# Kernel optimization log

Measured on AMD Instinct MI355X. Metric: run time of the kernel, lower is better.

Reference implementation:

```python
import jax, jax.numpy as jnp
import numpy as np

N, D, H, E = 50000, 64, 4, 400000
LN_EPS = 1e-5


def setup_inputs() -> dict:
    key = jax.random.key(0)
    ks = jax.random.split(key, 8)
    x = jax.random.normal(ks[0], (N, D), dtype=jnp.float32)
    edge_index = jax.random.randint(ks[1], (2, E), 0, N, dtype=jnp.int64)
    # nn.Linear(dim, dim*heads, bias=False): weight shape (H*D, D)
    W_lin = jax.random.normal(ks[2], (H * D, D), dtype=jnp.float32) * (1.0 / np.sqrt(D))
    attn_src = jax.random.normal(ks[3], (H, D), dtype=jnp.float32) * 0.1
    attn_dst = jax.random.normal(ks[4], (H, D), dtype=jnp.float32) * 0.1
    # nn.Linear(dim*heads, dim): weight (D, H*D), bias (D,)
    W_out = jax.random.normal(ks[5], (D, H * D), dtype=jnp.float32) * (1.0 / np.sqrt(H * D))
    b_out = jnp.zeros((D,), dtype=jnp.float32)
    ln_g = jnp.ones((D,), dtype=jnp.float32)
    ln_b = jnp.zeros((D,), dtype=jnp.float32)
    return {"x": x, "edge_index": edge_index, "W_lin": W_lin,
            "attn_src": attn_src, "attn_dst": attn_dst,
            "W_out": W_out, "b_out": b_out, "ln_g": ln_g, "ln_b": ln_b}


def reference(x, edge_index, W_lin, attn_src, attn_dst, W_out, b_out, ln_g, ln_b):
    n = x.shape[0]
    i, j = edge_index[0], edge_index[1]  # dst, src node ids per edge
    xh = (x @ W_lin.T).reshape(n, H, D)                 # [N,H,D]
    # per-node attention contributions (equivalent to per-edge dot in source)
    s_dst = jnp.einsum('nhd,hd->nh', xh, attn_dst)      # [N,H]
    s_src = jnp.einsum('nhd,hd->nh', xh, attn_src)      # [N,H]
    alpha = jax.nn.leaky_relu(s_dst[i] + s_src[j], 0.2) # [E,H]
    alpha_exp = jnp.exp(alpha)                          # source uses raw exp (no max-shift)
    denom = jax.ops.segment_sum(alpha_exp, i, num_segments=n)  # [N,H]
    attn = alpha_exp / (denom[i] + 1e-9)                # [E,H]
    msg = attn[:, :, None] * xh[j]                      # [E,H,D]
    out = jax.ops.segment_sum(msg, i, num_segments=n)   # [N,H,D]
    out = out.reshape(n, H * D) @ W_out.T + b_out       # [N,D]
    y = jax.nn.elu(out) + x
    mu = jnp.mean(y, axis=-1, keepdims=True)
    var = jnp.mean(jnp.square(y - mu), axis=-1, keepdims=True)
    return (y - mu) * jax.lax.rsqrt(var + LN_EPS) * ln_g + ln_b
```

## Files before the change

### kernel.cpp

```cpp
#include <hip/hip_runtime.h>

#define N_NODES 50000
#define DIM     64
#define HEADS   4
#define NEDGES  400000
#define HD      256
#define MAXDEG  32
#define NPREP   256
#define ZSTRIDE 264

typedef _Float16 half2v __attribute__((ext_vector_type(2)));
typedef _Float16 half4v __attribute__((ext_vector_type(4)));
typedef _Float16 half8v __attribute__((ext_vector_type(8)));
typedef float    f32x4  __attribute__((ext_vector_type(4)));

union EU { int2 i2; half4v h; };

__global__ __launch_bounds__(256) void k_prep(
    const float* __restrict__ x,
    const float* __restrict__ W_lin,
    const float* __restrict__ attn_src,
    const float* __restrict__ attn_dst,
    const float* __restrict__ W_out,
    const int* __restrict__ ei,
    _Float16* __restrict__ G2T,
    _Float16* __restrict__ x16,
    float* __restrict__ S,
    int* __restrict__ cnt,
    int* __restrict__ bucketJ)
{
    __shared__ float weffsh[512];
    const int b = blockIdx.x, t = threadIdx.x;

    for (int e = b * 256 + t; e < NEDGES; e += NPREP * 256) {
        const int i = ei[e];
        const int j = ei[NEDGES + e];
        const int slot = atomicAdd(&cnt[i], 1);
        if (slot < MAXDEG) bucketJ[(size_t)i * MAXDEG + slot] = j;
    }

    for (int id = t; id < 512; id += 256) {
        const int sd = id >> 8, rem = id & 255, h = rem >> 6, k = rem & 63;
        const float* av = sd ? attn_dst : attn_src;
        float acc = 0.f;
        for (int d = 0; d < DIM; ++d)
            acc = fmaf(av[h * DIM + d], W_lin[(h * DIM + d) * DIM + k], acc);
        weffsh[id] = acc;
    }

    {
        const int id = b * 256 + t;
        if (id < 64 * 256) {
            const int d = id >> 8, rem = id & 255, m = rem >> 2, h = rem & 3;
            float acc = 0.f;
            for (int k = 0; k < DIM; ++k)
                acc = fmaf(W_lin[(h * DIM + k) * DIM + m],
                           W_out[d * HD + h * DIM + k], acc);
            G2T[d * HD + m * 4 + h] = (_Float16)acc;
        }
    }
    __syncthreads();

    for (int base = b * 32; base < N_NODES; base += NPREP * 32) {
        const int ni = base + (t >> 3);
        if (ni < N_NODES) {
            const int combo = t & 7;
            const float4* xr = (const float4*)(x + (size_t)ni * DIM);
            const float4* wr = (const float4*)(weffsh + combo * DIM);
            float acc = 0.f;
#pragma unroll
            for (int kp = 0; kp < 16; ++kp) {
                const float4 a = xr[kp], bw = wr[kp];
                acc = fmaf(a.x, bw.x, acc);
                acc = fmaf(a.y, bw.y, acc);
                acc = fmaf(a.z, bw.z, acc);
                acc = fmaf(a.w, bw.w, acc);
            }
            S[(size_t)ni * 8 + combo] = acc;
        }
        const size_t e0 = (size_t)base * DIM + (size_t)t * 8;
        if (e0 + 8 <= (size_t)N_NODES * DIM) {
            const float4 u = *(const float4*)(x + e0);
            const float4 v = *(const float4*)(x + e0 + 4);
            half8v hv;
            hv[0]=(_Float16)u.x; hv[1]=(_Float16)u.y; hv[2]=(_Float16)u.z; hv[3]=(_Float16)u.w;
            hv[4]=(_Float16)v.x; hv[5]=(_Float16)v.y; hv[6]=(_Float16)v.z; hv[7]=(_Float16)v.w;
            *(half8v*)(x16 + e0) = hv;
        }
    }
}

__global__ __launch_bounds__(256) void k_ga(
    const int* __restrict__ cnt,
    const int* __restrict__ bucketJ,
    const float* __restrict__ S,
    const _Float16* __restrict__ x16,
    const _Float16* __restrict__ G2T,
    const float* __restrict__ b_out,
    const float* __restrict__ ln_g,
    const float* __restrict__ ln_b,
    float* __restrict__ out)
{
    __shared__ _Float16 znsh[16 * ZSTRIDE];
    __shared__ float ysh[16][65];

    const int t = threadIdx.x, wv = t >> 6, l = t & 63;
    const int n0 = blockIdx.x * 16;
    const int side = l >> 5, p = l & 31;

    const int4 degv = *(const int4*)(cnt + n0 + wv * 4);
    int degc[4];
    degc[0] = degv.x < MAXDEG ? degv.x : MAXDEG;
    degc[1] = degv.y < MAXDEG ? degv.y : MAXDEG;
    degc[2] = degv.z < MAXDEG ? degv.z : MAXDEG;
    degc[3] = degv.w < MAXDEG ? degv.w : MAXDEG;

    int Jr[4];
#pragma unroll
    for (int r = 0; r < 4; ++r)
        Jr[r] = bucketJ[(size_t)(n0 + wv * 4 + r) * MAXDEG + p];
#pragma unroll
    for (int r = 0; r < 4; ++r)
        Jr[r] = (p < degc[r]) ? Jr[r] : 0;

    float4 SSr[4], SDr[4];
#pragma unroll
    for (int r = 0; r < 4; ++r)
        SSr[r] = *(const float4*)(S + (size_t)Jr[r] * 8);
#pragma unroll
    for (int r = 0; r < 4; ++r)
        SDr[r] = *(const float4*)(S + (size_t)(n0 + wv * 4 + r) * 8 + 4);

    int Ey[4], Ez[4];
#pragma unroll
    for (int r = 0; r < 4; ++r) {
        float u;
        u = SDr[r].x + SSr[r].x; u = u > 0.f ? u : 0.2f * u; const float e0 = __expf(u);
        u = SDr[r].y + SSr[r].y; u = u > 0.f ? u : 0.2f * u; const float e1 = __expf(u);
        u = SDr[r].z + SSr[r].z; u = u > 0.f ? u : 0.2f * u; const float e2 = __expf(u);
        u = SDr[r].w + SSr[r].w; u = u > 0.f ? u : 0.2f * u; const float e3 = __expf(u);
        EU pk;
        pk.h[0] = (_Float16)e0; pk.h[1] = (_Float16)e1;
        pk.h[2] = (_Float16)e2; pk.h[3] = (_Float16)e3;
        Ey[r] = pk.i2.x; Ez[r] = pk.i2.y;
    }

    auto issue_group = [&](int r, int s, int deg, int* jjo, half2v* xvo) {
#pragma unroll
        for (int q = 0; q < 4; ++q) {
            const int ss = s + 2 * q + side;
            const int jv = __shfl(Jr[r], ss, 64);
            jjo[q] = (ss < deg) ? jv : 0;
        }
#pragma unroll
        for (int q = 0; q < 4; ++q)
            xvo[q] = *(const half2v*)(x16 + (size_t)jjo[q] * DIM + p * 2);
    };

    int jjc[4]; half2v xvc[4];
    issue_group(0, 0, degc[0], jjc, xvc);

#pragma unroll
    for (int r = 0; r < 4; ++r) {
        int jjn[4]; half2v xvn[4];
        if (r < 3) issue_group(r + 1, 0, degc[r + 1], jjn, xvn);

        float za[4] = {0.f, 0.f, 0.f, 0.f};
        float zb[4] = {0.f, 0.f, 0.f, 0.f};
        float dd[4] = {0.f, 0.f, 0.f, 0.f};

        auto consume_group = [&](int s, const half2v* xv) {
#pragma unroll
            for (int q = 0; q < 4; ++q) {
                const int ss = s + 2 * q + side;
                int ey = __shfl(Ey[r], ss, 64);
                int ez = __shfl(Ez[r], ss, 64);
                const bool v = ss < degc[r];
                ey = v ? ey : 0;
                ez = v ? ez : 0;
                EU u; u.i2 = make_int2(ey, ez);
                const float e0 = (float)u.h[0], e1 = (float)u.h[1];
                const float e2 = (float)u.h[2], e3 = (float)u.h[3];
                dd[0] += e0; dd[1] += e1; dd[2] += e2; dd[3] += e3;
                const float fa = (float)xv[q][0], fb = (float)xv[q][1];
                za[0] = fmaf(e0, fa, za[0]); za[1] = fmaf(e1, fa, za[1]);
                za[2] = fmaf(e2, fa, za[2]); za[3] = fmaf(e3, fa, za[3]);
                zb[0] = fmaf(e0, fb, zb[0]); zb[1] = fmaf(e1, fb, zb[1]);
                zb[2] = fmaf(e2, fb, zb[2]); zb[3] = fmaf(e3, fb, zb[3]);
            }
        };

        consume_group(0, xvc);
        for (int s = 8; s < degc[r]; s += 8) {
            int jr2[4]; half2v xr2[4];
            issue_group(r, s, degc[r], jr2, xr2);
            consume_group(s, xr2);
        }

#pragma unroll
        for (int h = 0; h < 4; ++h) {
            dd[h] += __shfl_xor(dd[h], 32, 64);
            za[h] += __shfl_xor(za[h], 32, 64);
            zb[h] += __shfl_xor(zb[h], 32, 64);
        }
        const float r0 = 1.f / (dd[0] + 1e-9f), r1 = 1.f / (dd[1] + 1e-9f);
        const float r2 = 1.f / (dd[2] + 1e-9f), r3 = 1.f / (dd[3] + 1e-9f);
        if (side == 0) {
            half8v o;
            o[0] = (_Float16)(za[0] * r0); o[1] = (_Float16)(za[1] * r1);
            o[2] = (_Float16)(za[2] * r2); o[3] = (_Float16)(za[3] * r3);
            o[4] = (_Float16)(zb[0] * r0); o[5] = (_Float16)(zb[1] * r1);
            o[6] = (_Float16)(zb[2] * r2); o[7] = (_Float16)(zb[3] * r3);
            *(half8v*)(znsh + (wv * 4 + r) * ZSTRIDE + p * 8) = o;
        }

#pragma unroll
        for (int q = 0; q < 4; ++q) { jjc[q] = jjn[q]; xvc[q] = xvn[q]; }
    }
    __syncthreads();

    const int mrow = l & 15, quad = l >> 4;
    half8v A[8];
    const _Float16* zr = znsh + mrow * ZSTRIDE + quad * 8;
#pragma unroll
    for (int s = 0; s < 8; ++s)
        A[s] = *(const half8v*)(zr + 32 * s);

    const _Float16* gp = G2T + (size_t)(wv * 16 + mrow) * HD + quad * 8;
    f32x4 c = {0.f, 0.f, 0.f, 0.f};
#pragma unroll
    for (int s = 0; s < 8; ++s)
        c = __builtin_amdgcn_mfma_f32_16x16x32_f16(A[s], *(const half8v*)(gp + 32 * s), c, 0, 0, 0);

    const int col = wv * 16 + mrow;
    const float bo = b_out[col];
#pragma unroll
    for (int rho = 0; rho < 4; ++rho) {
        const int nl = quad * 4 + rho;
        const float o = c[rho] + bo;
        const float eo = o > 0.f ? o : expm1f(o);
        ysh[nl][col] = eo + (float)x16[(size_t)(n0 + nl) * DIM + col];
    }
    __syncthreads();

    const float g = ln_g[l], bb = ln_b[l];
#pragma unroll
    for (int r = 0; r < 4; ++r) {
        const int nl = wv * 4 + r;
        const float y = ysh[nl][l];
        float sum = y;
#pragma unroll
        for (int off = 32; off > 0; off >>= 1) sum += __shfl_xor(sum, off, 64);
        const float mu = sum * (1.f / 64.f);
        const float dy = y - mu;
        float vs = dy * dy;
#pragma unroll
        for (int off = 32; off > 0; off >>= 1) vs += __shfl_xor(vs, off, 64);
        const float rr = rsqrtf(vs * (1.f / 64.f) + 1e-5f);
        out[(size_t)(n0 + nl) * DIM + l] = dy * rr * g + bb;
    }
}

extern "C" void kernel_launch(void* const* d_in, const int* in_sizes, int n_in,
                              void* d_out, int out_size, void* d_ws, size_t ws_size,
                              hipStream_t stream)
{
    const float* x        = (const float*)d_in[0];
    const int*   ei       = (const int*)d_in[1];
    const float* W_lin    = (const float*)d_in[2];
    const float* attn_src = (const float*)d_in[3];
    const float* attn_dst = (const float*)d_in[4];
    const float* W_out    = (const float*)d_in[5];
    const float* b_out    = (const float*)d_in[6];
    const float* ln_g     = (const float*)d_in[7];
    const float* ln_b     = (const float*)d_in[8];
    float* out = (float*)d_out;

    char* ws = (char*)d_ws;
    _Float16* x16    = (_Float16*)ws;
    float*    S      = (float*)(x16 + (size_t)N_NODES * DIM);
    _Float16* G2T    = (_Float16*)(S + (size_t)N_NODES * 8);
    int*      cnt    = (int*)(G2T + 64 * HD);
    int*      bucketJ= cnt + N_NODES;

    hipMemsetAsync(cnt, 0, (size_t)N_NODES * sizeof(int), stream);

    k_prep<<<NPREP, 256, 0, stream>>>(x, W_lin, attn_src, attn_dst, W_out, ei,
                                      G2T, x16, S, cnt, bucketJ);

    k_ga<<<N_NODES / 16, 256, 0, stream>>>(cnt, bucketJ, S, x16, G2T,
                                           b_out, ln_g, ln_b, out);
}
```

Before: 157.0 us.

## Use fp16 dot2 accumulation with LDS-staged edge weights in gather-aggregate

Replaces the per-edge shuffles of packed exp weights with LDS staging, so each lane reads its weights directly. Edges are paired and packed with v_perm, and the weighted sums and denominators are accumulated with fdot2 instructions, which roughly halves the FMA count. It also prefetches the second group of 8 edges ahead of time, uses the fast rcp intrinsic, and switches to 32-bit index math. It depends on zeroed weights for padded edges, which changes how masking is done, and fdot2 may differ slightly in rounding.

```diff
diff --git a/kernel.cpp b/kernel.cpp
--- a/kernel.cpp
+++ b/kernel.cpp
@@ -9,12 +9,25 @@
 #define NPREP   256
 #define ZSTRIDE 264
 
+#define USE_DOT2 1
+
 typedef _Float16 half2v __attribute__((ext_vector_type(2)));
 typedef _Float16 half4v __attribute__((ext_vector_type(4)));
 typedef _Float16 half8v __attribute__((ext_vector_type(8)));
 typedef float    f32x4  __attribute__((ext_vector_type(4)));
 
 union EU { int2 i2; half4v h; };
+union HU { unsigned int u; half2v h; };
+
+__device__ __forceinline__ half2v h2cast(unsigned int u) { HU c; c.u = u; return c.h; }
+
+#if USE_DOT2
+#define DOT2(a, b, c) __builtin_amdgcn_fdot2((a), (b), (c), false)
+#else
+__device__ __forceinline__ float DOT2(half2v a, half2v b, float c) {
+    return fmaf((float)a[1], (float)b[1], fmaf((float)a[0], (float)b[0], c));
+}
+#endif
 
 __global__ __launch_bounds__(256) void k_prep(
     const float* __restrict__ x,
@@ -103,6 +116,7 @@
 {
     __shared__ _Float16 znsh[16 * ZSTRIDE];
     __shared__ float ysh[16][65];
+    __shared__ int2  esh[16 * 32];
 
     const int t = threadIdx.x, wv = t >> 6, l = t & 63;
     const int n0 = blockIdx.x * 16;
@@ -118,7 +132,7 @@
     int Jr[4];
 #pragma unroll
     for (int r = 0; r < 4; ++r)
-        Jr[r] = bucketJ[(size_t)(n0 + wv * 4 + r) * MAXDEG + p];
+        Jr[r] = bucketJ[(unsigned)(n0 + wv * 4 + r) * MAXDEG + p];
 #pragma unroll
     for (int r = 0; r < 4; ++r)
         Jr[r] = (p < degc[r]) ? Jr[r] : 0;
@@ -126,12 +140,11 @@
     float4 SSr[4], SDr[4];
 #pragma unroll
     for (int r = 0; r < 4; ++r)
-        SSr[r] = *(const float4*)(S + (size_t)Jr[r] * 8);
+        SSr[r] = *(const float4*)(S + (unsigned)Jr[r] * 8);
 #pragma unroll
     for (int r = 0; r < 4; ++r)
-        SDr[r] = *(const float4*)(S + (size_t)(n0 + wv * 4 + r) * 8 + 4);
-
-    int Ey[4], Ez[4];
+        SDr[r] = *(const float4*)(S + (unsigned)(n0 + wv * 4 + r) * 8 + 4);
+
 #pragma unroll
     for (int r = 0; r < 4; ++r) {
         float u;
@@ -142,59 +155,72 @@
         EU pk;
         pk.h[0] = (_Float16)e0; pk.h[1] = (_Float16)e1;
         pk.h[2] = (_Float16)e2; pk.h[3] = (_Float16)e3;
-        Ey[r] = pk.i2.x; Ez[r] = pk.i2.y;
-    }
-
-    auto issue_group = [&](int r, int s, int deg, int* jjo, half2v* xvo) {
+        int2 ev = pk.i2;
+        if (p >= degc[r]) { ev.x = 0; ev.y = 0; }
+        if (side == 0) esh[(wv * 4 + r) * 32 + p] = ev;
+    }
+    __builtin_amdgcn_wave_barrier();
+
+    struct Grp { half2v xv[4]; int2 ee[4]; };
+    float za[4], zb[4], dd[4];
+    const half2v one2 = h2cast(0x3C003C00u);
+
+    auto stage_group = [&](int r, int s, Grp& g) {
+        const int jb = s + side;
 #pragma unroll
         for (int q = 0; q < 4; ++q) {
-            const int ss = s + 2 * q + side;
-            const int jv = __shfl(Jr[r], ss, 64);
-            jjo[q] = (ss < deg) ? jv : 0;
-        }
+            const int jv = __shfl(Jr[r], jb + 2 * q, 64);
+            g.xv[q] = *(const half2v*)(x16 + (unsigned)jv * DIM + (p << 1));
+        }
+        const int eb = (wv * 4 + r) * 32 + jb;
 #pragma unroll
         for (int q = 0; q < 4; ++q)
-            xvo[q] = *(const half2v*)(x16 + (size_t)jjo[q] * DIM + p * 2);
+            g.ee[q] = esh[eb + 2 * q];
     };
 
-    int jjc[4]; half2v xvc[4];
-    issue_group(0, 0, degc[0], jjc, xvc);
+    auto consume_group = [&](const Grp& g) {
+#pragma unroll
+        for (int pp = 0; pp < 2; ++pp) {
+            const int2 ea = g.ee[2 * pp], eb2 = g.ee[2 * pp + 1];
+            HU xa, xb; xa.h = g.xv[2 * pp]; xb.h = g.xv[2 * pp + 1];
+            const unsigned E0 = __builtin_amdgcn_perm(eb2.x, ea.x, 0x05040100u);
+            const unsigned E1 = __builtin_amdgcn_perm(eb2.x, ea.x, 0x07060302u);
+            const unsigned E2 = __builtin_amdgcn_perm(eb2.y, ea.y, 0x05040100u);
+            const unsigned E3 = __builtin_amdgcn_perm(eb2.y, ea.y, 0x07060302u);
+            const unsigned XA = __builtin_amdgcn_perm(xb.u, xa.u, 0x05040100u);
+            const unsigned XB = __builtin_amdgcn_perm(xb.u, xa.u, 0x07060302u);
+            const half2v f0 = h2cast(E0), f1 = h2cast(E1);
+            const half2v f2 = h2cast(E2), f3 = h2cast(E3);
+            const half2v va = h2cast(XA), vb = h2cast(XB);
+            za[0] = DOT2(f0, va, za[0]); za[1] = DOT2(f1, va, za[1]);
+            za[2] = DOT2(f2, va, za[2]); za[3] = DOT2(f3, va, za[3]);
+            zb[0] = DOT2(f0, vb, zb[0]); zb[1] = DOT2(f1, vb, zb[1]);
+            zb[2] = DOT2(f2, vb, zb[2]); zb[3] = DOT2(f3, vb, zb[3]);
+            dd[0] = DOT2(f0, one2, dd[0]); dd[1] = DOT2(f1, one2, dd[1]);
+            dd[2] = DOT2(f2, one2, dd[2]); dd[3] = DOT2(f3, one2, dd[3]);
+        }
+    };
+
+    Grp cur, nxt, remb;
+    stage_group(0, 0, cur);
 
 #pragma unroll
     for (int r = 0; r < 4; ++r) {
-        int jjn[4]; half2v xvn[4];
-        if (r < 3) issue_group(r + 1, 0, degc[r + 1], jjn, xvn);
-
-        float za[4] = {0.f, 0.f, 0.f, 0.f};
-        float zb[4] = {0.f, 0.f, 0.f, 0.f};
-        float dd[4] = {0.f, 0.f, 0.f, 0.f};
-
-        auto consume_group = [&](int s, const half2v* xv) {
-#pragma unroll
-            for (int q = 0; q < 4; ++q) {
-                const int ss = s + 2 * q + side;
-                int ey = __shfl(Ey[r], ss, 64);
-                int ez = __shfl(Ez[r], ss, 64);
-                const bool v = ss < degc[r];
-                ey = v ? ey : 0;
-                ez = v ? ez : 0;
-                EU u; u.i2 = make_int2(ey, ez);
-                const float e0 = (float)u.h[0], e1 = (float)u.h[1];
-                const float e2 = (float)u.h[2], e3 = (float)u.h[3];
-                dd[0] += e0; dd[1] += e1; dd[2] += e2; dd[3] += e3;
-                const float fa = (float)xv[q][0], fb = (float)xv[q][1];
-                za[0] = fmaf(e0, fa, za[0]); za[1] = fmaf(e1, fa, za[1]);
-                za[2] = fmaf(e2, fa, za[2]); za[3] = fmaf(e3, fa, za[3]);
-                zb[0] = fmaf(e0, fb, zb[0]); zb[1] = fmaf(e1, fb, zb[1]);
-                zb[2] = fmaf(e2, fb, zb[2]); zb[3] = fmaf(e3, fb, zb[3]);
+        const bool rem = degc[r] > 8;
+        if (rem) stage_group(r, 8, remb);
+        if (r < 3) stage_group(r + 1, 0, nxt);
+
+#pragma unroll
+        for (int h = 0; h < 4; ++h) { za[h] = 0.f; zb[h] = 0.f; dd[h] = 0.f; }
+
+        consume_group(cur);
+        if (rem) {
+            consume_group(remb);
+            for (int s = 16; s < degc[r]; s += 8) {
+                Grp tg;
+                stage_group(r, s, tg);
+                consume_group(tg);
             }
-        };
-
-        consume_group(0, xvc);
-        for (int s = 8; s < degc[r]; s += 8) {
-            int jr2[4]; half2v xr2[4];
-            issue_group(r, s, degc[r], jr2, xr2);
-            consume_group(s, xr2);
         }
 
 #pragma unroll
@@ -203,8 +229,10 @@
             za[h] += __shfl_xor(za[h], 32, 64);
             zb[h] += __shfl_xor(zb[h], 32, 64);
         }
-        const float r0 = 1.f / (dd[0] + 1e-9f), r1 = 1.f / (dd[1] + 1e-9f);
-        const float r2 = 1.f / (dd[2] + 1e-9f), r3 = 1.f / (dd[3] + 1e-9f);
+        const float r0 = __builtin_amdgcn_rcpf(dd[0] + 1e-9f);
+        const float r1 = __builtin_amdgcn_rcpf(dd[1] + 1e-9f);
+        const float r2 = __builtin_amdgcn_rcpf(dd[2] + 1e-9f);
+        const float r3 = __builtin_amdgcn_rcpf(dd[3] + 1e-9f);
         if (side == 0) {
             half8v o;
             o[0] = (_Float16)(za[0] * r0); o[1] = (_Float16)(za[1] * r1);
@@ -213,9 +241,7 @@
             o[6] = (_Float16)(zb[2] * r2); o[7] = (_Float16)(zb[3] * r3);
             *(half8v*)(znsh + (wv * 4 + r) * ZSTRIDE + p * 8) = o;
         }
-
-#pragma unroll
-        for (int q = 0; q < 4; ++q) { jjc[q] = jjn[q]; xvc[q] = xvn[q]; }
+        cur = nxt;
     }
     __syncthreads();
 
```

After: 149.6 us. 4.7% less time.
